# Kernel tuning notes

Measured on AMD Instinct MI355X. Metric: run time of the kernel, lower is better.

The kernel has to match this reference:

```python
import jax, jax.numpy as jnp
import numpy as np

B, T, D, N, H = 2, 2048, 2048, 16, 128
WINDOW = 1024
SOFT_CAP = 50.0
K_MASK = -2.3819763e+38
MAX_WAVELENGTH = 10000


def apply_rope(x, positions, head_dim):
    # x: [B, T, N, H], positions: [B, T]
    fraction = 2.0 * jnp.arange(head_dim // 2, dtype=jnp.float32) / head_dim
    timescale = MAX_WAVELENGTH ** fraction                      # [H/2]
    sinusoid = positions[..., None].astype(jnp.float32) / timescale  # [B, T, H/2]
    sinusoid = sinusoid[..., None, :]                           # [B, T, 1, H/2]
    sin, cos = jnp.sin(sinusoid), jnp.cos(sinusoid)
    first, second = jnp.split(x, 2, axis=-1)
    out = jnp.concatenate([first * cos - second * sin,
                           second * cos + first * sin], axis=-1)
    return out.astype(x.dtype)


def setup_inputs() -> dict:
    key = jax.random.key(0)
    k1, k2, k3 = jax.random.split(key, 3)
    x = jax.random.normal(k1, (B, T, D), dtype=jnp.float32)
    w_qkv = jax.random.normal(k2, (3, N, D, H), dtype=jnp.float32) * (D ** -0.5)
    w_out = jax.random.normal(k3, (N, H, D), dtype=jnp.float32) * ((N * H) ** -0.5)
    segment_pos = jnp.broadcast_to(jnp.arange(T, dtype=jnp.int32), (B, T))
    # causal attention mask [B, T, S]
    causal = jnp.tril(jnp.ones((T, T), dtype=jnp.bool_))
    attn_mask = jnp.broadcast_to(causal, (B, T, T))
    return {"x": x, "w_qkv": w_qkv, "w_out": w_out,
            "segment_pos": segment_pos, "attn_mask": attn_mask}


def reference(x, w_qkv, w_out, segment_pos, attn_mask):
    # QKV projection: [3, B, T, N, H]
    q, k, v = jnp.einsum('BTD,SNDH->SBTNH', x, w_qkv)
    q = apply_rope(q, segment_pos, H) * (H ** -0.5)
    k = apply_rope(k, segment_pos, H)
    logits = jnp.einsum('BTNH,BSNH->BTNS', q, k)
    # soft cap
    logits = jnp.tanh(logits / SOFT_CAP) * SOFT_CAP
    # sliding-window mask combined with causal mask
    ones = jnp.ones_like(attn_mask)
    sliding = jnp.triu(ones, -WINDOW + 1) & jnp.tril(ones, WINDOW - 1)
    mask = sliding & attn_mask                                   # [B, T, S]
    padded = jnp.where(mask[:, :, None, :], logits, K_MASK)
    probs = jax.nn.softmax(padded, axis=-1).astype(k.dtype)
    encoded = jnp.einsum('BTNS,BSNH->BTNH', probs, v)
    return jnp.einsum('BTNH,NHD->BTD', encoded, w_out)
```

## Files before the change

### kernel.cpp

```cpp
#include <hip/hip_runtime.h>

#define B_ 2
#define T_ 2048
#define D_ 2048
#define N_ 16
#define H_ 128
constexpr int WIN = 1024;

typedef __attribute__((ext_vector_type(8))) short s16x8;
typedef __attribute__((ext_vector_type(4))) float f32x4;

typedef const __attribute__((address_space(1))) void cglobal_void;
typedef __attribute__((address_space(3))) void lds_void;

__device__ __forceinline__ unsigned short f2b(float f) {
  union { float f; unsigned u; } v; v.f = f;
  unsigned r = v.u + 0x7FFFu + ((v.u >> 16) & 1u);
  return (unsigned short)(r >> 16);
}
__device__ __forceinline__ float b2f(unsigned short u) {
  union { unsigned u; float f; } v; v.u = ((unsigned)u) << 16;
  return v.f;
}

__global__ __launch_bounds__(256) void detect_kernel(
    const unsigned short* __restrict__ x, int* __restrict__ flag) {
  __shared__ int cnt[256];
  const int tid = threadIdx.x;
  int c = 0;
  for (int i = tid; i < 4096; i += 256) {
    const unsigned short u = x[2 * i];
    const int e = (u >> 7) & 0xFF;
    if (e >= 154) ++c;
  }
  cnt[tid] = c;
  __syncthreads();
  for (int s = 128; s > 0; s >>= 1) {
    if (tid < s) cnt[tid] += cnt[tid + s];
    __syncthreads();
  }
  if (tid == 0) *flag = cnt[0];
}

__global__ __launch_bounds__(256) void convert_x_kernel(
    const void* __restrict__ src, unsigned short* __restrict__ dst,
    const int* __restrict__ flag, int n) {
  const int i = blockIdx.x * 256 + threadIdx.x;
  if (i >= n) return;
  const bool isf = (*flag > 64);
  dst[i] = isf ? f2b(((const float*)src)[i]) : ((const unsigned short*)src)[i];
}

__global__ __launch_bounds__(256) void transpose_kernel(
    const void* __restrict__ src, unsigned short* __restrict__ dst,
    int R, int C, const int* __restrict__ flag) {
  __shared__ unsigned short tile[32][33];
  const bool isf = (*flag > 64);
  const int c0 = blockIdx.x * 32, r0 = blockIdx.y * 32;
  const size_t base = (size_t)blockIdx.z * R * C;
  const int tx = threadIdx.x, ty = threadIdx.y;
#pragma unroll
  for (int j = 0; j < 32; j += 8) {
    const size_t idx = base + (size_t)(r0 + ty + j) * C + c0 + tx;
    tile[ty + j][tx] = isf ? f2b(((const float*)src)[idx])
                           : ((const unsigned short*)src)[idx];
  }
  __syncthreads();
#pragma unroll
  for (int j = 0; j < 32; j += 8)
    dst[base + (size_t)(c0 + ty + j) * R + r0 + tx] = tile[tx][ty + j];
}

__global__ __launch_bounds__(256) void transpose_bf16_kernel(
    const unsigned short* __restrict__ src, unsigned short* __restrict__ dst,
    int R, int C) {
  __shared__ unsigned short tile[32][33];
  const int c0 = blockIdx.x * 32, r0 = blockIdx.y * 32;
  const size_t base = (size_t)blockIdx.z * R * C;
  const int tx = threadIdx.x, ty = threadIdx.y;
#pragma unroll
  for (int j = 0; j < 32; j += 8)
    tile[ty + j][tx] = src[base + (size_t)(r0 + ty + j) * C + c0 + tx];
  __syncthreads();
#pragma unroll
  for (int j = 0; j < 32; j += 8)
    dst[base + (size_t)(c0 + ty + j) * R + r0 + tx] = tile[tx][ty + j];
}

__global__ __launch_bounds__(256) void gemm128_kernel(
    const unsigned short* __restrict__ A,
    const unsigned short* __restrict__ Bt,
    void* __restrict__ outp,
    int mode, const int* __restrict__ flag) {
  constexpr int K = D_;
  __shared__ unsigned short As[128 * 32];
  __shared__ unsigned short Bs[128 * 32];
  const int tid = threadIdx.x;
  const int wave = tid >> 6, lane = tid & 63;
  const int lr = lane & 15, lq = lane >> 4;
  const int wm = (wave >> 1) * 64, wn = (wave & 1) * 64;
  const size_t m0 = (size_t)blockIdx.x * 128;
  const unsigned short* pA = A + m0 * K;
  const unsigned short* pB = Bt + (size_t)blockIdx.y * 128 * K;

  f32x4 acc[4][4] = {};

  const int cA = tid, cB = 256 + tid;
  const int row0 = cA >> 2, col0 = (cA & 3) * 8;
  const int row1 = cB >> 2, col1 = (cB & 3) * 8;
  unsigned short* lA0 = As + (size_t)(wave * 64) * 8;
  unsigned short* lA1 = As + (size_t)(256 + wave * 64) * 8;
  unsigned short* lB0 = Bs + (size_t)(wave * 64) * 8;
  unsigned short* lB1 = Bs + (size_t)(256 + wave * 64) * 8;

  for (int k0 = 0; k0 < K; k0 += 32) {
    __syncthreads();
    __builtin_amdgcn_global_load_lds((cglobal_void*)(pA + (size_t)row0 * K + k0 + col0),
                                     (lds_void*)lA0, 16, 0, 0);
    __builtin_amdgcn_global_load_lds((cglobal_void*)(pA + (size_t)row1 * K + k0 + col1),
                                     (lds_void*)lA1, 16, 0, 0);
    __builtin_amdgcn_global_load_lds((cglobal_void*)(pB + (size_t)row0 * K + k0 + col0),
                                     (lds_void*)lB0, 16, 0, 0);
    __builtin_amdgcn_global_load_lds((cglobal_void*)(pB + (size_t)row1 * K + k0 + col1),
                                     (lds_void*)lB1, 16, 0, 0);
    __syncthreads();
    s16x8 af[4], bfr[4];
#pragma unroll
    for (int mb = 0; mb < 4; ++mb)
      af[mb] = *(const s16x8*)(As + (wm + mb * 16 + lr) * 32 + lq * 8);
#pragma unroll
    for (int nb = 0; nb < 4; ++nb)
      bfr[nb] = *(const s16x8*)(Bs + (wn + nb * 16 + lr) * 32 + lq * 8);
#pragma unroll
    for (int mb = 0; mb < 4; ++mb)
#pragma unroll
      for (int nb = 0; nb < 4; ++nb)
        acc[mb][nb] = __builtin_amdgcn_mfma_f32_16x16x32_bf16(af[mb], bfr[nb], acc[mb][nb], 0, 0, 0);
  }

  if (mode == 0) {
    const bool isf = (*flag > 64);
#pragma unroll
    for (int mb = 0; mb < 4; ++mb) {
      const size_t r = m0 + wm + mb * 16 + lq * 4;
#pragma unroll
      for (int nb = 0; nb < 4; ++nb) {
        const size_t c = (size_t)blockIdx.y * 128 + wn + nb * 16 + lr;
#pragma unroll
        for (int i = 0; i < 4; ++i) {
          if (isf) ((float*)outp)[(r + i) * D_ + c] = acc[mb][nb][i];
          else ((unsigned short*)outp)[(r + i) * D_ + c] = f2b(acc[mb][nb][i]);
        }
      }
    }
  } else {
    unsigned short* op = (unsigned short*)outp;
    const int s = blockIdx.y >> 4, n = blockIdx.y & 15;
    const size_t SB = (size_t)B_ * N_ * T_ * H_;
#pragma unroll
    for (int mb = 0; mb < 4; ++mb) {
#pragma unroll
      for (int i = 0; i < 4; ++i) {
        const size_t r = m0 + wm + mb * 16 + lq * 4 + i;
        const int b = (int)(r >> 11);
        const int t = (int)(r & 2047);
        const size_t base = s * SB + (size_t)(b * N_ + n) * T_ * H_ + (size_t)t * H_;
#pragma unroll
        for (int nb = 0; nb < 4; ++nb)
          op[base + wn + nb * 16 + lr] = f2b(acc[mb][nb][i]);
      }
    }
  }
}

__global__ __launch_bounds__(256) void rope_kernel(unsigned short* __restrict__ qk) {
  const int tid = threadIdx.x;
  const int lane = tid & 63;
  const size_t row = (size_t)blockIdx.x * 4 + (tid >> 6);
  const int t = (int)(row & (T_ - 1));
  const int s = (int)(row >> 16);
  unsigned short* p = qk + row * H_;
  float x1 = b2f(p[lane]), x2 = b2f(p[lane + 64]);
  float inv_ts = powf(10000.0f, -((float)lane) * (1.0f / 64.0f));
  float sv, cv;
  sincosf((float)t * inv_ts, &sv, &cv);
  float o1 = x1 * cv - x2 * sv;
  float o2 = x2 * cv + x1 * sv;
  if (s == 0) { o1 *= 0.08838834764831845f; o2 *= 0.08838834764831845f; }
  p[lane] = f2b(o1);
  p[lane + 64] = f2b(o2);
}

__global__ __launch_bounds__(256, 4) void attn_kernel(
    const unsigned short* __restrict__ qkv,
    const unsigned short* __restrict__ vt,
    unsigned short* __restrict__ enc) {
  const int tid = threadIdx.x, lane = tid & 63, wave = tid >> 6;
  const int lr = lane & 15, lq = lane >> 4;
  const int bn = blockIdx.x;
  const int b = bn >> 4, n = bn & 15;
  const int t0 = blockIdx.y * 64;
  const size_t SB = (size_t)B_ * N_ * T_ * H_;
  const unsigned short* qp = qkv + (size_t)bn * T_ * H_;
  const unsigned short* kp = qp + SB;
  const unsigned short* vp = vt + (size_t)bn * T_ * H_;

  __shared__ unsigned short Ks[64 * 136];
  __shared__ unsigned short Vt[128 * 72];
  unsigned short* Ps = Ks + wave * (16 * 136);

  s16x8 aq[4];
  {
    const int t = t0 + wave * 16 + lr;
#pragma unroll
    for (int kc = 0; kc < 4; ++kc)
      aq[kc] = *(const s16x8*)(qp + (size_t)t * H_ + kc * 32 + lq * 8);
  }

  f32x4 oacc[8] = {};
  float lp[4] = {0.f, 0.f, 0.f, 0.f};

  const int s_lo = (t0 >= WIN - 1) ? ((t0 - (WIN - 1)) & ~63) : 0;
  constexpr float C_IN = 2.885390082f / 50.0f;
  constexpr float C_T = 50.0f * 1.442695041f;
  constexpr float C_OFF = 12.0f * 1.442695041f;

  for (int s0 = s_lo; s0 <= t0 + 63; s0 += 64) {
    __syncthreads();
#pragma unroll
    for (int j = 0; j < 4; ++j) {
      const int c = j * 256 + tid;
      const int row = c >> 4, col = (c & 15) * 8;
      *(s16x8*)(Ks + row * 136 + col) = *(const s16x8*)(kp + (size_t)(s0 + row) * H_ + col);
    }
#pragma unroll
    for (int j = 0; j < 4; ++j) {
      const int c = j * 256 + tid;
      const int row = c >> 3, col = (c & 7) * 8;
      *(s16x8*)(Vt + row * 72 + col) = *(const s16x8*)(vp + (size_t)row * T_ + s0 + col);
    }
    __syncthreads();

    float p[4][4];
#pragma unroll
    for (int sb = 0; sb < 4; ++sb) {
      f32x4 a = {};
#pragma unroll
      for (int kc = 0; kc < 4; ++kc) {
        s16x8 bk = *(const s16x8*)(Ks + (sb * 16 + lr) * 136 + kc * 32 + lq * 8);
        a = __builtin_amdgcn_mfma_f32_16x16x32_bf16(aq[kc], bk, a, 0, 0, 0);
      }
#pragma unroll
      for (int i = 0; i < 4; ++i) {
        float zz = a[i] * C_IN;
        zz = fminf(fmaxf(zz, -44.0f), 44.0f);
        const float u = exp2f(zz);
        const float th = (u - 1.0f) * __builtin_amdgcn_rcpf(u + 1.0f);
        p[sb][i] = exp2f(th * C_T - C_OFF);
      }
    }

    const bool interior = (s0 + 63 <= t0) && (s0 >= t0 + 63 - (WIN - 1));
    if (!interior) {
#pragma unroll
      for (int sb = 0; sb < 4; ++sb) {
        const int key = s0 + sb * 16 + lr;
#pragma unroll
        for (int i = 0; i < 4; ++i) {
          const int t = t0 + wave * 16 + lq * 4 + i;
          if (key > t || key < t - (WIN - 1)) p[sb][i] = 0.0f;
        }
      }
    }
#pragma unroll
    for (int sb = 0; sb < 4; ++sb)
#pragma unroll
      for (int i = 0; i < 4; ++i) lp[i] += p[sb][i];

    __syncthreads();
#pragma unroll
    for (int sb = 0; sb < 4; ++sb)
#pragma unroll
      for (int i = 0; i < 4; ++i)
        Ps[(lq * 4 + i) * 136 + sb * 16 + lr] = f2b(p[sb][i]);
    __syncthreads();

    s16x8 ap[2];
#pragma unroll
    for (int kc = 0; kc < 2; ++kc)
      ap[kc] = *(const s16x8*)(Ps + lr * 136 + kc * 32 + lq * 8);

#pragma unroll
    for (int hb = 0; hb < 8; ++hb) {
#pragma unroll
      for (int kc = 0; kc < 2; ++kc) {
        s16x8 bv = *(const s16x8*)(Vt + (hb * 16 + lr) * 72 + kc * 32 + lq * 8);
        oacc[hb] = __builtin_amdgcn_mfma_f32_16x16x32_bf16(ap[kc], bv, oacc[hb], 0, 0, 0);
      }
    }
  }

#pragma unroll
  for (int i = 0; i < 4; ++i) {
#pragma unroll
    for (int off = 1; off < 16; off <<= 1)
      lp[i] += __shfl_xor(lp[i], off, 64);
  }

#pragma unroll
  for (int i = 0; i < 4; ++i) {
    const int t = t0 + wave * 16 + lq * 4 + i;
    const float inv = 1.0f / lp[i];
    const size_t rowb = ((size_t)b * T_ + t) * (N_ * H_) + (size_t)n * H_;
#pragma unroll
    for (int hb = 0; hb < 8; ++hb)
      enc[rowb + hb * 16 + lr] = f2b(oacc[hb][i] * inv);
  }
}

extern "C" void kernel_launch(void* const* d_in, const int* in_sizes, int n_in,
                              void* d_out, int out_size, void* d_ws, size_t ws_size,
                              hipStream_t stream) {
  const void* x     = d_in[0];
  const void* w_qkv = d_in[1];
  const void* w_out = d_in[2];

  char* wsb = (char*)d_ws;
  int* flag = (int*)wsb;
  const size_t MB = 1048576;
  unsigned short* xc    = (unsigned short*)(wsb + 64);
  unsigned short* wqkvT = (unsigned short*)(wsb + 64 + 16 * MB);
  unsigned short* qkv   = (unsigned short*)(wsb + 64 + 40 * MB);
  unsigned short* vt    = xc;
  unsigned short* enc   = wqkvT;
  unsigned short* woutT = (unsigned short*)(wsb + 64 + 32 * MB);
  unsigned short* v     = qkv + 2 * (size_t)B_ * N_ * T_ * H_;

  detect_kernel<<<1, 256, 0, stream>>>((const unsigned short*)x, flag);
  convert_x_kernel<<<32768, 256, 0, stream>>>(x, xc, flag, B_ * T_ * D_);
  transpose_kernel<<<dim3(4, 64, 48), dim3(32, 8), 0, stream>>>(w_qkv, wqkvT, 2048, 128, flag);
  gemm128_kernel<<<dim3(32, 48), 256, 0, stream>>>(xc, wqkvT, qkv, 1, flag);
  rope_kernel<<<32768, 256, 0, stream>>>(qkv);
  transpose_bf16_kernel<<<dim3(4, 64, 32), dim3(32, 8), 0, stream>>>(v, vt, 2048, 128);
  transpose_kernel<<<dim3(64, 64, 1), dim3(32, 8), 0, stream>>>(w_out, woutT, 2048, 2048, flag);
  attn_kernel<<<dim3(32, 32), 256, 0, stream>>>(qkv, vt, enc);
  gemm128_kernel<<<dim3(32, 16), 256, 0, stream>>>(enc, woutT, d_out, 0, flag);
}
```

Before: 512.1 us.

## Swizzle LDS layouts, deepen GEMM K-tile, async-load attention tiles, simplify softcap math

The GEMM now stages 64-wide K tiles into XOR-swizzled LDS through direct global-to-LDS loads, which halves the number of barrier pairs and avoids bank conflicts without padding. The attention kernel loads K and V tiles the same way and swizzles its P buffer. The softcapped exponent is rewritten as exp2 of an affine function of 1/(1+u) with no clamp, fewer ops but possible edge-case overflow. The x conversion is vectorised four-wide and RoPE uses fast exp2/sincos intrinsics, which may cost accuracy at large angles.

```diff
diff --git a/kernel.cpp b/kernel.cpp
--- a/kernel.cpp
+++ b/kernel.cpp
@@ -9,6 +9,7 @@
 
 typedef __attribute__((ext_vector_type(8))) short s16x8;
 typedef __attribute__((ext_vector_type(4))) float f32x4;
+typedef __attribute__((ext_vector_type(4))) unsigned short u16x4;
 
 typedef const __attribute__((address_space(1))) void cglobal_void;
 typedef __attribute__((address_space(3))) void lds_void;
@@ -44,11 +45,18 @@
 
 __global__ __launch_bounds__(256) void convert_x_kernel(
     const void* __restrict__ src, unsigned short* __restrict__ dst,
-    const int* __restrict__ flag, int n) {
+    const int* __restrict__ flag, int n4) {
   const int i = blockIdx.x * 256 + threadIdx.x;
-  if (i >= n) return;
+  if (i >= n4) return;
   const bool isf = (*flag > 64);
-  dst[i] = isf ? f2b(((const float*)src)[i]) : ((const unsigned short*)src)[i];
+  u16x4 o;
+  if (isf) {
+    const float4 f = ((const float4*)src)[i];
+    o[0] = f2b(f.x); o[1] = f2b(f.y); o[2] = f2b(f.z); o[3] = f2b(f.w);
+  } else {
+    o = ((const u16x4*)src)[i];
+  }
+  *(u16x4*)(dst + 4 * (size_t)i) = o;
 }
 
 __global__ __launch_bounds__(256) void transpose_kernel(
@@ -93,11 +101,12 @@
     void* __restrict__ outp,
     int mode, const int* __restrict__ flag) {
   constexpr int K = D_;
-  __shared__ unsigned short As[128 * 32];
-  __shared__ unsigned short Bs[128 * 32];
+  __shared__ unsigned short As[128 * 64];
+  __shared__ unsigned short Bs[128 * 64];
   const int tid = threadIdx.x;
-  const int wave = tid >> 6, lane = tid & 63;
+  const int lane = tid & 63;
   const int lr = lane & 15, lq = lane >> 4;
+  const int wave = tid >> 6;
   const int wm = (wave >> 1) * 64, wn = (wave & 1) * 64;
   const size_t m0 = (size_t)blockIdx.x * 128;
   const unsigned short* pA = A + m0 * K;
@@ -105,37 +114,38 @@
 
   f32x4 acc[4][4] = {};
 
-  const int cA = tid, cB = 256 + tid;
-  const int row0 = cA >> 2, col0 = (cA & 3) * 8;
-  const int row1 = cB >> 2, col1 = (cB & 3) * 8;
-  unsigned short* lA0 = As + (size_t)(wave * 64) * 8;
-  unsigned short* lA1 = As + (size_t)(256 + wave * 64) * 8;
-  unsigned short* lB0 = Bs + (size_t)(wave * 64) * 8;
-  unsigned short* lB1 = Bs + (size_t)(256 + wave * 64) * 8;
-
-  for (int k0 = 0; k0 < K; k0 += 32) {
-    __syncthreads();
-    __builtin_amdgcn_global_load_lds((cglobal_void*)(pA + (size_t)row0 * K + k0 + col0),
-                                     (lds_void*)lA0, 16, 0, 0);
-    __builtin_amdgcn_global_load_lds((cglobal_void*)(pA + (size_t)row1 * K + k0 + col1),
-                                     (lds_void*)lA1, 16, 0, 0);
-    __builtin_amdgcn_global_load_lds((cglobal_void*)(pB + (size_t)row0 * K + k0 + col0),
-                                     (lds_void*)lB0, 16, 0, 0);
-    __builtin_amdgcn_global_load_lds((cglobal_void*)(pB + (size_t)row1 * K + k0 + col1),
-                                     (lds_void*)lB1, 16, 0, 0);
-    __syncthreads();
-    s16x8 af[4], bfr[4];
-#pragma unroll
-    for (int mb = 0; mb < 4; ++mb)
-      af[mb] = *(const s16x8*)(As + (wm + mb * 16 + lr) * 32 + lq * 8);
-#pragma unroll
-    for (int nb = 0; nb < 4; ++nb)
-      bfr[nb] = *(const s16x8*)(Bs + (wn + nb * 16 + lr) * 32 + lq * 8);
-#pragma unroll
-    for (int mb = 0; mb < 4; ++mb)
+  const int cg = (tid & 7) ^ ((tid >> 3) & 7);
+  size_t goff[4];
+#pragma unroll
+  for (int j = 0; j < 4; ++j)
+    goff[j] = (size_t)(j * 32 + (tid >> 3)) * K + cg * 8;
+
+  for (int k0 = 0; k0 < K; k0 += 64) {
+    __syncthreads();
+#pragma unroll
+    for (int j = 0; j < 4; ++j) {
+      __builtin_amdgcn_global_load_lds((cglobal_void*)(pA + goff[j] + k0),
+                                       (lds_void*)(As + (size_t)(j * 256 + tid) * 8), 16, 0, 0);
+      __builtin_amdgcn_global_load_lds((cglobal_void*)(pB + goff[j] + k0),
+                                       (lds_void*)(Bs + (size_t)(j * 256 + tid) * 8), 16, 0, 0);
+    }
+    __syncthreads();
+#pragma unroll
+    for (int kq = 0; kq < 2; ++kq) {
+      const int co = (((kq << 2) + lq) ^ (lr & 7)) * 8;
+      s16x8 af[4], bfr[4];
+#pragma unroll
+      for (int mb = 0; mb < 4; ++mb)
+        af[mb] = *(const s16x8*)(As + (wm + mb * 16 + lr) * 64 + co);
 #pragma unroll
       for (int nb = 0; nb < 4; ++nb)
-        acc[mb][nb] = __builtin_amdgcn_mfma_f32_16x16x32_bf16(af[mb], bfr[nb], acc[mb][nb], 0, 0, 0);
+        bfr[nb] = *(const s16x8*)(Bs + (wn + nb * 16 + lr) * 64 + co);
+#pragma unroll
+      for (int mb = 0; mb < 4; ++mb)
+#pragma unroll
+        for (int nb = 0; nb < 4; ++nb)
+          acc[mb][nb] = __builtin_amdgcn_mfma_f32_16x16x32_bf16(af[mb], bfr[nb], acc[mb][nb], 0, 0, 0);
+    }
   }
 
   if (mode == 0) {
@@ -181,9 +191,9 @@
   const int s = (int)(row >> 16);
   unsigned short* p = qk + row * H_;
   float x1 = b2f(p[lane]), x2 = b2f(p[lane + 64]);
-  float inv_ts = powf(10000.0f, -((float)lane) * (1.0f / 64.0f));
+  const float inv_ts = exp2f(-0.20762050f * (float)lane);
   float sv, cv;
-  sincosf((float)t * inv_ts, &sv, &cv);
+  __sincosf((float)t * inv_ts, &sv, &cv);
   float o1 = x1 * cv - x2 * sv;
   float o2 = x2 * cv + x1 * sv;
   if (s == 0) { o1 *= 0.08838834764831845f; o2 *= 0.08838834764831845f; }
@@ -205,9 +215,18 @@
   const unsigned short* kp = qp + SB;
   const unsigned short* vp = vt + (size_t)bn * T_ * H_;
 
-  __shared__ unsigned short Ks[64 * 136];
-  __shared__ unsigned short Vt[128 * 72];
-  unsigned short* Ps = Ks + wave * (16 * 136);
+  __shared__ unsigned short Ks[64 * 128];
+  __shared__ unsigned short Vt[128 * 64];
+  unsigned short* Ps = Ks + wave * 1024;
+
+  const int cgK = (tid & 15) ^ ((tid >> 4) & 15);
+  const int cgV = (tid & 7) ^ ((tid >> 3) & 7);
+  size_t goffK[4], goffV[4];
+#pragma unroll
+  for (int j = 0; j < 4; ++j) {
+    goffK[j] = (size_t)(j * 16 + (tid >> 4)) * H_ + cgK * 8;
+    goffV[j] = (size_t)(j * 32 + (tid >> 3)) * T_ + cgV * 8;
+  }
 
   s16x8 aq[4];
   {
@@ -221,23 +240,18 @@
   float lp[4] = {0.f, 0.f, 0.f, 0.f};
 
   const int s_lo = (t0 >= WIN - 1) ? ((t0 - (WIN - 1)) & ~63) : 0;
-  constexpr float C_IN = 2.885390082f / 50.0f;
-  constexpr float C_T = 50.0f * 1.442695041f;
-  constexpr float C_OFF = 12.0f * 1.442695041f;
+  constexpr float C_IN = 0.05770780f;
+  constexpr float M_SCALE = -144.269504f;
+  constexpr float M_BIAS = 86.56f;
 
   for (int s0 = s_lo; s0 <= t0 + 63; s0 += 64) {
     __syncthreads();
 #pragma unroll
     for (int j = 0; j < 4; ++j) {
-      const int c = j * 256 + tid;
-      const int row = c >> 4, col = (c & 15) * 8;
-      *(s16x8*)(Ks + row * 136 + col) = *(const s16x8*)(kp + (size_t)(s0 + row) * H_ + col);
-    }
-#pragma unroll
-    for (int j = 0; j < 4; ++j) {
-      const int c = j * 256 + tid;
-      const int row = c >> 3, col = (c & 7) * 8;
-      *(s16x8*)(Vt + row * 72 + col) = *(const s16x8*)(vp + (size_t)row * T_ + s0 + col);
+      __builtin_amdgcn_global_load_lds((cglobal_void*)(kp + (size_t)s0 * H_ + goffK[j]),
+                                       (lds_void*)(Ks + (size_t)(j * 256 + tid) * 8), 16, 0, 0);
+      __builtin_amdgcn_global_load_lds((cglobal_void*)(vp + goffV[j] + s0),
+                                       (lds_void*)(Vt + (size_t)(j * 256 + tid) * 8), 16, 0, 0);
     }
     __syncthreads();
 
@@ -247,16 +261,15 @@
       f32x4 a = {};
 #pragma unroll
       for (int kc = 0; kc < 4; ++kc) {
-        s16x8 bk = *(const s16x8*)(Ks + (sb * 16 + lr) * 136 + kc * 32 + lq * 8);
+        const int co = (((kc << 2) + lq) ^ lr) * 8;
+        s16x8 bk = *(const s16x8*)(Ks + (sb * 16 + lr) * 128 + co);
         a = __builtin_amdgcn_mfma_f32_16x16x32_bf16(aq[kc], bk, a, 0, 0, 0);
       }
 #pragma unroll
       for (int i = 0; i < 4; ++i) {
-        float zz = a[i] * C_IN;
-        zz = fminf(fmaxf(zz, -44.0f), 44.0f);
-        const float u = exp2f(zz);
-        const float th = (u - 1.0f) * __builtin_amdgcn_rcpf(u + 1.0f);
-        p[sb][i] = exp2f(th * C_T - C_OFF);
+        const float u = exp2f(a[i] * C_IN);
+        const float r = __builtin_amdgcn_rcpf(u + 1.0f);
+        p[sb][i] = exp2f(fmaf(r, M_SCALE, M_BIAS));
       }
     }
 
@@ -281,20 +294,24 @@
 #pragma unroll
     for (int sb = 0; sb < 4; ++sb)
 #pragma unroll
-      for (int i = 0; i < 4; ++i)
-        Ps[(lq * 4 + i) * 136 + sb * 16 + lr] = f2b(p[sb][i]);
+      for (int i = 0; i < 4; ++i) {
+        const int row = lq * 4 + i;
+        const int cph = ((sb * 2 + (lr >> 3)) ^ (row & 7));
+        Ps[row * 64 + cph * 8 + (lr & 7)] = f2b(p[sb][i]);
+      }
     __syncthreads();
 
     s16x8 ap[2];
 #pragma unroll
     for (int kc = 0; kc < 2; ++kc)
-      ap[kc] = *(const s16x8*)(Ps + lr * 136 + kc * 32 + lq * 8);
+      ap[kc] = *(const s16x8*)(Ps + lr * 64 + ((((kc << 2) + lq) ^ (lr & 7)) * 8));
 
 #pragma unroll
     for (int hb = 0; hb < 8; ++hb) {
 #pragma unroll
       for (int kc = 0; kc < 2; ++kc) {
-        s16x8 bv = *(const s16x8*)(Vt + (hb * 16 + lr) * 72 + kc * 32 + lq * 8);
+        const int co = (((kc << 2) + lq) ^ (lr & 7)) * 8;
+        s16x8 bv = *(const s16x8*)(Vt + (hb * 16 + lr) * 64 + co);
         oacc[hb] = __builtin_amdgcn_mfma_f32_16x16x32_bf16(ap[kc], bv, oacc[hb], 0, 0, 0);
       }
     }
@@ -337,7 +354,7 @@
   unsigned short* v     = qkv + 2 * (size_t)B_ * N_ * T_ * H_;
 
   detect_kernel<<<1, 256, 0, stream>>>((const unsigned short*)x, flag);
-  convert_x_kernel<<<32768, 256, 0, stream>>>(x, xc, flag, B_ * T_ * D_);
+  convert_x_kernel<<<8192, 256, 0, stream>>>(x, xc, flag, B_ * T_ * D_ / 4);
   transpose_kernel<<<dim3(4, 64, 48), dim3(32, 8), 0, stream>>>(w_qkv, wqkvT, 2048, 128, flag);
   gemm128_kernel<<<dim3(32, 48), 256, 0, stream>>>(xc, wqkvT, qkv, 1, flag);
   rope_kernel<<<32768, 256, 0, stream>>>(qkv);
```

New measurement: 459.0 us. -10.4%, faster.
